# Optimization experiments

Measured on AMD Instinct MI355X. Metric: run time of the kernel, lower is better.

## Reference

```python
import jax, jax.numpy as jnp
import numpy as np

B, T, K, U, C, M, H = 64, 600, 10, 64, 54, 20, 512
OUT = 1 + 6 * M        # 121
IN1 = 3 + C            # 57  -> rnn_cell1 input
IN2 = 3 + C + H        # 569 -> rnn_cell2 input
BIAS = 0.0
EPS = 1e-20


def setup_inputs() -> dict:
    key = jax.random.key(0)
    ks = jax.random.split(key, 20)
    p = lambda k, shape: (jax.random.normal(k, shape, dtype=jnp.float32) * 0.05)
    return {
        "x": jax.random.normal(ks[0], (B, T, 3), dtype=jnp.float32),
        "y": jax.random.uniform(ks[1], (B, T, 3), dtype=jnp.float32),
        "c_vec": jax.random.uniform(ks[2], (B, U, C), dtype=jnp.float32),
        "W_ih1": p(ks[3], (4 * H, IN1)), "W_hh1": p(ks[4], (4 * H, H)),
        "b_ih1": p(ks[5], (4 * H,)),     "b_hh1": p(ks[6], (4 * H,)),
        "W_ih2": p(ks[7], (4 * H, IN2)), "W_hh2": p(ks[8], (4 * H, H)),
        "b_ih2": p(ks[9], (4 * H,)),     "b_hh2": p(ks[10], (4 * H,)),
        "W_k": p(ks[11], (3 * K, H)),    "b_k": p(ks[12], (3 * K,)),
        "W_o": p(ks[13], (OUT, H)),      "b_o": p(ks[14], (OUT,)),
    }


def _lstm_cell(xin, h, c, Wih, Whh, bih, bhh):
    g = xin @ Wih.T + h @ Whh.T + bih + bhh          # [B, 4H]
    i, f, gg, o = jnp.split(g, 4, axis=1)            # PyTorch LSTMCell gate order
    c = jax.nn.sigmoid(f) * c + jax.nn.sigmoid(i) * jnp.tanh(gg)
    h = jax.nn.sigmoid(o) * jnp.tanh(c)
    return h, c


def _forward(x, y, c_vec, W_ih1, W_hh1, b_ih1, b_hh1, W_ih2, W_hh2, b_ih2, b_hh2,
             W_k, b_k, W_o, b_o):
    u = jnp.arange(U, dtype=jnp.float32)[None, None, :]   # [1,1,U]
    zB = jnp.zeros((B, H), dtype=x.dtype)

    def step(carry, xt):
        h1, c1, h2, c2, w, kappa = carry
        h1, c1 = _lstm_cell(jnp.concatenate([xt, w], 1), h1, c1, W_ih1, W_hh1, b_ih1, b_hh1)
        kg = h1 @ W_k.T + b_k                               # [B, 3K]
        a_hat, be_hat, ka_hat = jnp.split(kg, 3, axis=1)
        alpha = jnp.exp(a_hat)[:, :, None]                  # [B,K,1]
        beta = jnp.exp(be_hat)[:, :, None]
        kappa = kappa + jnp.exp(ka_hat)[:, :, None]
        phi = jnp.sum(jnp.exp(-beta * (kappa - u) ** 2) * alpha, axis=1)  # [B,U]
        w = jnp.einsum('bu,buc->bc', phi, c_vec)            # [B,C]
        h2, c2 = _lstm_cell(jnp.concatenate([xt, h1, w], 1), h2, c2, W_ih2, W_hh2, b_ih2, b_hh2)
        return (h1, c1, h2, c2, w, kappa), h2

    init = (zB, zB, zB, zB, jnp.zeros((B, C), x.dtype), jnp.zeros((B, K, 1), x.dtype))
    _, h2_seq = jax.lax.scan(step, init, jnp.transpose(x, (1, 0, 2)))   # [T,B,H]
    h2_seq = jnp.transpose(h2_seq, (1, 0, 2)).reshape(-1, H)            # [B*T,H]
    outputs = h2_seq @ W_o.T + b_o                                      # [B*T,OUT]

    y1, y2, s = jnp.moveaxis(y.reshape(-1, 3), 1, 0)                    # each [B*T]
    e = jax.nn.sigmoid(-outputs[:, 0])                                  # 1/(1+exp(o0))
    pi_hat, mu1, mu2, s1_hat, s2_hat, rho_hat = jnp.split(outputs[:, 1:], 6, axis=1)
    pi = jax.nn.softmax(pi_hat, axis=1)
    sigma1 = jnp.exp(s1_hat - BIAS)
    sigma2 = jnp.exp(s2_hat - BIAS)
    rho = jnp.tanh(rho_hat)
    d1 = (y1[:, None] - mu1) / sigma1
    d2 = (y2[:, None] - mu2) / sigma2
    z = d1 ** 2 + d2 ** 2 - 2.0 * rho * d1 * d2
    one_m_r2 = 1.0 - rho ** 2
    gauss = jnp.exp(-z / (2.0 * one_m_r2)) / (2.0 * np.pi * sigma1 * sigma2 * jnp.sqrt(one_m_r2))
    loss_g = jnp.sum(-jnp.log(jnp.sum(pi * gauss, axis=1) + EPS))
    loss_b = jnp.sum(-jnp.log((e + EPS) * s + (1.0 - e + EPS) * (1.0 - s)))
    return (loss_g + loss_b) / (B * T)


def reference(x, y, c_vec, W_ih1, W_hh1, b_ih1, b_hh1, W_ih2, W_hh2, b_ih2, b_hh2,
              W_k, b_k, W_o, b_o):
    return _forward(x, y, c_vec, W_ih1, W_hh1, b_ih1, b_hh1, W_ih2, W_hh2,
                    b_ih2, b_hh2, W_k, b_k, W_o, b_o)
```

## Files before the change

### kernel.cpp

```cpp
#include <hip/hip_runtime.h>
#include <math.h>

typedef _Float16 f16;
typedef _Float16 f16x8 __attribute__((ext_vector_type(8)));
typedef float f32x4 __attribute__((ext_vector_type(4)));
union HU { f16 h; unsigned short u; };

#define NT 512
#define NBLK 160
#define ABE 69632
#define OUTG_OFF 69632
#define LOSS_OFF 77824
#define FLAG_OFF 78080
#define DYN_LDS 132096

__device__ __forceinline__ f16x8 cld16(const void* p) {
  f16x8 r;
  asm volatile("global_load_dwordx4 %0, %1, off sc0 sc1" : "=v"(r) : "v"(p) : "memory");
  return r;
}
__device__ __forceinline__ uint4 cld128u(const void* p) {
  uint4 r;
  asm volatile("global_load_dwordx4 %0, %1, off sc0 sc1"
               : "=v"(r) : "v"(p) : "memory");
  return r;
}
__device__ __forceinline__ unsigned cld32u(const void* p) {
  unsigned r;
  asm volatile("global_load_dword %0, %1, off sc0 sc1" : "=v"(r) : "v"(p) : "memory");
  return r;
}
__device__ __forceinline__ void cst32(void* p, unsigned v) {
  asm volatile("global_store_dword %0, %1, off sc0 sc1" :: "v"(p), "v"(v) : "memory");
}
#define VMWAIT() do { asm volatile("s_waitcnt vmcnt(0)" ::: "memory"); \
                      __builtin_amdgcn_sched_barrier(0); } while (0)

__device__ __forceinline__ float sigm(float v){ return 1.f/(1.f+expf(-v)); }

__device__ __forceinline__ void gbar(unsigned* flags, unsigned target) {
  asm volatile("s_waitcnt vmcnt(0)" ::: "memory");
  __syncthreads();
  if (threadIdx.x == 0) cst32(flags + blockIdx.x, target);
  if (threadIdx.x < 64) {
    bool ok;
    do {
      uint4 vv; vv.x = vv.y = vv.z = vv.w = target;
      if (threadIdx.x < 40) {
        vv = cld128u(flags + threadIdx.x * 4);
        asm volatile("s_waitcnt vmcnt(0)" ::: "memory");
      }
      ok = (vv.x >= target) && (vv.y >= target) && (vv.z >= target) && (vv.w >= target);
    } while (!__all(ok));
  }
  __syncthreads();
}

__device__ __forceinline__ float mix_loss(const float* so, const float* yl, int t, int m) {
  float y1 = yl[t*3+0], y2 = yl[t*3+1], ys = yl[t*3+2];
  float ph = (m < 20) ? so[1+m] : -1e30f;
  float mx = ph;
  #pragma unroll
  for (int d = 16; d >= 1; d >>= 1) mx = fmaxf(mx, __shfl_xor(mx, d));
  float pe = (m < 20) ? expf(ph - mx) : 0.f;
  float ps = pe;
  #pragma unroll
  for (int d = 16; d >= 1; d >>= 1) ps += __shfl_xor(ps, d);
  float contrib = 0.f;
  if (m < 20) {
    float mu1 = so[21+m], mu2 = so[41+m];
    float s1 = expf(so[61+m]), s2 = expf(so[81+m]);
    float rh = tanhf(so[101+m]);
    float d1 = (y1-mu1)/s1, d2 = (y2-mu2)/s2;
    float omr = 1.f - rh*rh;
    float z = d1*d1 + d2*d2 - 2.f*rh*d1*d2;
    float ga = expf(-z/(2.f*omr)) / (6.283185307179586f * s1 * s2 * sqrtf(omr));
    contrib = (pe/ps)*ga;
  }
  float gs = contrib;
  #pragma unroll
  for (int d = 16; d >= 1; d >>= 1) gs += __shfl_xor(gs, d);
  float lg = -logf(gs + 1e-20f);
  float e = 1.f/(1.f + expf(so[0]));
  float lb = -logf((e + 1e-20f)*ys + (1.f - e + 1e-20f)*(1.f - ys));
  return lg + lb;
}

__global__ __launch_bounds__(256) void k_init(float* ws) {
  unsigned* w0 = (unsigned*)ws;
  unsigned* wb = (unsigned*)ws + FLAG_OFF;
  int idx = blockIdx.x*256 + threadIdx.x;
  int str = gridDim.x*256;
  for (int e = idx; e < ABE; e += str) w0[e] = 0u;
  if (idx < NBLK) wb[idx] = 0u;
}

__global__ __launch_bounds__(NT, 1) void kmain(
    const float* __restrict__ x, const float* __restrict__ y, const float* __restrict__ cvec,
    const float* __restrict__ Wih1, const float* __restrict__ Whh1,
    const float* __restrict__ bih1, const float* __restrict__ bhh1,
    const float* __restrict__ Wih2, const float* __restrict__ Whh2,
    const float* __restrict__ bih2, const float* __restrict__ bhh2,
    const float* __restrict__ Wk, const float* __restrict__ bk,
    const float* __restrict__ Wo, const float* __restrict__ bo,
    float* __restrict__ out, float* __restrict__ ws)
{
  extern __shared__ char dsm[];
  const int blk = blockIdx.x, tid = threadIdx.x;
  const int wv = tid >> 6, l = tid & 63;

  f16* AB = (f16*)ws;
  float* outg  = ws + OUTG_OFF;
  float* lossg = ws + LOSS_OFF;
  unsigned* flags = (unsigned*)ws + FLAG_OFF;

  float lreg = 0.f;

  if (blk < 64) {
    f16* wf2 = (f16*)dsm;
    for (int f = tid; f < 2*34*64; f += NT) {
      int nt = f / (34*64), rem = f - nt*34*64, j = rem >> 6, lf = rem & 63;
      int nrow = nt*16 + (lf & 15);
      int R = (nrow >> 3)*512 + blk*8 + (nrow & 7);
      int kbase = j*32 + (lf >> 4)*8;
      #pragma unroll
      for (int e = 0; e < 8; ++e) {
        int k = kbase + e;
        float v = 0.f;
        if (k >= 4 && k < 58)        v = Wih2[R*569 + 515 + (k-4)];
        else if (k >= 58 && k < 61)  v = Wih2[R*569 + (k-58)];
        else if (k >= 64 && k < 576) v = Wih2[R*569 + 3 + (k-64)];
        else if (k >= 576)           v = Whh2[R*512 + (k-576)];
        wf2[f*8 + e] = (f16)v;
      }
    }
  } else if (blk < 96) {
    const int g1i = blk - 64;
    f16* wf1  = (f16*)dsm;
    f16* wofr = (f16*)(dsm + 73728);
    for (int f = tid; f < 4*18*64; f += NT) {
      int nt = f / (18*64), rem = f - nt*18*64, j = rem >> 6, lf = rem & 63;
      int nrow = nt*16 + (lf & 15);
      int R = (nrow >> 4)*512 + g1i*16 + (nrow & 15);
      int kbase = j*32 + (lf >> 4)*8;
      #pragma unroll
      for (int e = 0; e < 8; ++e) {
        int k = kbase + e;
        float v = 0.f;
        if (k < 3)                   v = Wih1[R*57 + k];
        else if (k >= 4 && k < 58)   v = Wih1[R*57 + 3 + (k-4)];
        else if (k >= 64 && k < 576) v = Whh1[R*512 + (k-64)];
        wf1[f*8 + e] = (f16)v;
      }
    }
    for (int f = tid; f < 16*64; f += NT) {
      int j = f >> 6, lf = f & 63;
      int nrow = lf & 15, row = g1i*4 + nrow;
      int kbase = j*32 + (lf >> 4)*8;
      #pragma unroll
      for (int e = 0; e < 8; ++e) {
        float v = (nrow < 4 && row < 121) ? Wo[row*512 + kbase + e] : 0.f;
        wofr[f*8 + e] = (f16)v;
      }
    }
  } else {
    const int b = blk - 96;
    f16*   wk  = (f16*)dsm;
    float* cv  = (float*)(dsm + 31200);
    float* xl  = (float*)(dsm + 45024);
    float* yl  = (float*)(dsm + 52224);
    for (int e = tid; e < 30*512; e += NT) { int j = e >> 9, k = e & 511; wk[j*520 + k] = (f16)Wk[e]; }
    for (int e = tid; e < 3456; e += NT) cv[e] = cvec[b*3456 + e];
    for (int e = tid; e < 1800; e += NT) { xl[e] = x[b*1800+e]; yl[e] = y[b*1800+e]; }
    float* kap = (float*)(dsm + 61152);
    if (tid < 10) kap[tid] = 0.f;
    __syncthreads();
    if (tid == 0) {
      HU h0, h1u, h2u;
      h0.h = (f16)xl[0]; h1u.h = (f16)xl[1]; h2u.h = (f16)xl[2];
      cst32((unsigned*)AB + (b*1088 >> 1),       (unsigned)h0.u | ((unsigned)h1u.u << 16));
      cst32((unsigned*)AB + ((b*1088 + 2) >> 1), (unsigned)h2u.u);
    }
  }

  float bias_g[4] = {0,0,0,0}, bias1a[4] = {0,0,0,0}, bias1b[4] = {0,0,0,0};
  float borow = 0.f;
  float c_st = 0.f, c1a = 0.f, c1b = 0.f;
  if (blk < 64) {
    int pr = tid & 7;
    #pragma unroll
    for (int g = 0; g < 4; ++g) {
      int R = g*512 + blk*8 + pr;
      bias_g[g] = bih2[R] + bhh2[R];
    }
  } else if (blk < 96) {
    int g1i = blk - 64, pr = tid & 7;
    #pragma unroll
    for (int g = 0; g < 4; ++g) {
      int Ra = g*512 + g1i*16 + 2*pr, Rb = Ra + 1;
      bias1a[g] = bih1[Ra] + bhh1[Ra];
      bias1b[g] = bih1[Rb] + bhh1[Rb];
    }
    int r = tid >> 6;
    if (r < 4) { int row = g1i*4 + r; borow = (row < 121) ? bo[row] : 0.f; }
  }

  gbar(flags, 1);

  for (int i = 0; i <= 601; ++i) {
    const f16* __restrict__ Acur = AB + (i & 1)*ABE;
    f16* __restrict__ Anxt = AB + ((i & 1)^1)*ABE;
    unsigned* AnxtW = (unsigned*)Anxt;

    if (blk < 64) {
      if (i >= 1 && i <= 600) {
        f16* wf2 = (f16*)dsm;
        float* part2 = (float*)(dsm + 69632);
        const int mt = wv & 3, kh = wv >> 2;
        const int mA = mt*16 + (l & 15);
        const int kb = (l >> 4)*8;
        const f16* Ap = Acur + mA*1088;
        f32x4 acc0 = {0,0,0,0}, acc1 = {0,0,0,0};
        f16x8 fr[17];
        #pragma unroll
        for (int jj = 0; jj < 17; ++jj) {
          int j = kh*17 + jj;
          fr[jj] = cld16(Ap + j*32 + kb);
        }
        VMWAIT();
        #pragma unroll
        for (int jj = 0; jj < 17; ++jj) {
          int j = kh*17 + jj;
          f16x8 b0 = *(const f16x8*)&wf2[((0*34 + j)*64 + l)*8];
          f16x8 b1 = *(const f16x8*)&wf2[((1*34 + j)*64 + l)*8];
          acc0 = __builtin_amdgcn_mfma_f32_16x16x32_f16(fr[jj], b0, acc0, 0, 0, 0);
          acc1 = __builtin_amdgcn_mfma_f32_16x16x32_f16(fr[jj], b1, acc1, 0, 0, 0);
        }
        #pragma unroll
        for (int r = 0; r < 4; ++r) {
          int m = mt*16 + (l>>4)*4 + r;
          part2[(kh*64 + m)*33 + (l & 15)]      = acc0[r];
          part2[(kh*64 + m)*33 + 16 + (l & 15)] = acc1[r];
        }
        __syncthreads();
        {
          int b_ = tid >> 3, pr = tid & 7;
          const float* p0 = &part2[(0*64 + b_)*33];
          const float* p1 = &part2[(1*64 + b_)*33];
          float gi_ = p0[0*8+pr] + p1[0*8+pr] + bias_g[0];
          float gf_ = p0[1*8+pr] + p1[1*8+pr] + bias_g[1];
          float gg_ = p0[2*8+pr] + p1[2*8+pr] + bias_g[2];
          float go_ = p0[3*8+pr] + p1[3*8+pr] + bias_g[3];
          float ig = sigm(gi_), fg = sigm(gf_), gg2 = tanhf(gg_), og = sigm(go_);
          c_st = fg*c_st + ig*gg2;
          HU hu; hu.h = (f16)(og * tanhf(c_st));
          unsigned myv = hu.u;
          unsigned other = (unsigned)__shfl_xor((int)myv, 1);
          if ((pr & 1) == 0)
            cst32(AnxtW + ((b_*1088 + 576 + blk*8 + pr) >> 1), myv | (other << 16));
        }
      }
    } else if (blk < 96) {
      const int g1i = blk - 64;
      f16* wf1  = (f16*)dsm;
      f16* wofr = (f16*)(dsm + 73728);
      float* part1 = (float*)(dsm + 90112);
      float* partp = (float*)(dsm + 123392);
      bool do_g1 = (i <= 599), do_pr = (i >= 2);
      const int mt = wv & 3, kh = wv >> 2;
      const int mA = mt*16 + (l & 15);
      const int kb = (l >> 4)*8;
      f16x8 fr1[9], frp[8];
      if (do_g1) {
        const f16* Ap = Acur + mA*1088;
        #pragma unroll
        for (int jj = 0; jj < 9; ++jj) {
          int j = kh*9 + jj;
          fr1[jj] = cld16(Ap + j*32 + kb);
        }
      }
      if (do_pr) {
        const f16* Ap = Acur + mA*1088 + 576;
        #pragma unroll
        for (int jj = 0; jj < 8; ++jj) {
          int j = kh*8 + jj;
          frp[jj] = cld16(Ap + j*32 + kb);
        }
      }
      VMWAIT();
      if (do_g1) {
        f32x4 acc[4];
        #pragma unroll
        for (int nt = 0; nt < 4; ++nt) acc[nt] = (f32x4){0,0,0,0};
        #pragma unroll
        for (int jj = 0; jj < 9; ++jj) {
          int j = kh*9 + jj;
          #pragma unroll
          for (int nt = 0; nt < 4; ++nt) {
            f16x8 bf = *(const f16x8*)&wf1[((nt*18 + j)*64 + l)*8];
            acc[nt] = __builtin_amdgcn_mfma_f32_16x16x32_f16(fr1[jj], bf, acc[nt], 0, 0, 0);
          }
        }
        #pragma unroll
        for (int nt = 0; nt < 4; ++nt)
          #pragma unroll
          for (int r = 0; r < 4; ++r) {
            int m = mt*16 + (l>>4)*4 + r;
            part1[(kh*64 + m)*65 + nt*16 + (l & 15)] = acc[nt][r];
          }
      }
      if (do_pr) {
        f32x4 accp = {0,0,0,0};
        #pragma unroll
        for (int jj = 0; jj < 8; ++jj) {
          int j = kh*8 + jj;
          f16x8 bf = *(const f16x8*)&wofr[(j*64 + l)*8];
          accp = __builtin_amdgcn_mfma_f32_16x16x32_f16(frp[jj], bf, accp, 0, 0, 0);
        }
        #pragma unroll
        for (int r = 0; r < 4; ++r) {
          int m = mt*16 + (l>>4)*4 + r;
          partp[(kh*64 + m)*17 + (l & 15)] = accp[r];
        }
      }
      if (do_g1 || do_pr) __syncthreads();
      if (do_g1) {
        int b_ = tid >> 3, pr = tid & 7;
        const float* p0 = &part1[(0*64 + b_)*65];
        const float* p1 = &part1[(1*64 + b_)*65];
        float giA = p0[0*16+2*pr] + p1[0*16+2*pr] + bias1a[0];
        float gfA = p0[1*16+2*pr] + p1[1*16+2*pr] + bias1a[1];
        float ggA = p0[2*16+2*pr] + p1[2*16+2*pr] + bias1a[2];
        float goA = p0[3*16+2*pr] + p1[3*16+2*pr] + bias1a[3];
        c1a = sigm(gfA)*c1a + sigm(giA)*tanhf(ggA);
        float hA = sigm(goA) * tanhf(c1a);
        float giB = p0[0*16+2*pr+1] + p1[0*16+2*pr+1] + bias1b[0];
        float gfB = p0[1*16+2*pr+1] + p1[1*16+2*pr+1] + bias1b[1];
        float ggB = p0[2*16+2*pr+1] + p1[2*16+2*pr+1] + bias1b[2];
        float goB = p0[3*16+2*pr+1] + p1[3*16+2*pr+1] + bias1b[3];
        c1b = sigm(gfB)*c1b + sigm(giB)*tanhf(ggB);
        float hB = sigm(goB) * tanhf(c1b);
        HU ua, ub; ua.h = (f16)hA; ub.h = (f16)hB;
        cst32(AnxtW + ((b_*1088 + 64 + g1i*16 + 2*pr) >> 1),
              (unsigned)ua.u | ((unsigned)ub.u << 16));
      }
      if (do_pr && tid < 256) {
        int b_ = tid & 63, r = tid >> 6;
        int row = g1i*4 + r;
        if (row < 121) {
          float v = partp[(0*64 + b_)*17 + r] + partp[(1*64 + b_)*17 + r] + borow;
          unsigned uu; __builtin_memcpy(&uu, &v, 4);
          cst32((unsigned*)outg + b_*128 + row, uu);
        }
      }
    }
    gbar(flags, 2 + 2*i);

    if (blk >= 96) {
      const int b = blk - 96;
      f16*   wk   = (f16*)dsm;
      float* cv   = (float*)(dsm + 31200);
      float* xl   = (float*)(dsm + 45024);
      float* yl   = (float*)(dsm + 52224);
      f16*   h1h  = (f16*)(dsm + 59424);
      float* so   = (float*)(dsm + 60448);
      float* skg  = (float*)(dsm + 60944);
      float* sal  = (float*)(dsm + 61072);
      float* sbe  = (float*)(dsm + 61112);
      float* kap  = (float*)(dsm + 61152);
      float* sphi = (float*)(dsm + 61192);
      float* wtmp = (float*)(dsm + 61448);
      if (i <= 599) {
        if (tid < 64) {
          f16x8 hv = cld16(Anxt + b*1088 + 64 + tid*8);
          asm volatile("s_waitcnt vmcnt(0)" ::: "memory");
          *(f16x8*)&h1h[tid*8] = hv;
        }
        __syncthreads();
        {
          int j = tid >> 4, ksv = tid & 15;
          float a = 0.f;
          if (j < 30) {
            const f16* wr = &wk[j*520 + ksv*32];
            const f16* hr = &h1h[ksv*32];
            #pragma unroll
            for (int c = 0; c < 4; ++c) {
              f16x8 q = *(const f16x8*)(wr + c*8);
              f16x8 h = *(const f16x8*)(hr + c*8);
              #pragma unroll
              for (int e = 0; e < 8; ++e) a += (float)q[e] * (float)h[e];
            }
          }
          a += __shfl_xor(a, 1); a += __shfl_xor(a, 2);
          a += __shfl_xor(a, 4); a += __shfl_xor(a, 8);
          if (j < 30 && ksv == 0) skg[j] = a + bk[j];
        }
        __syncthreads();
        if (tid < 10) {
          sal[tid] = expf(skg[tid]);
          sbe[tid] = expf(skg[10+tid]);
          kap[tid] += expf(skg[20+tid]);
        }
        __syncthreads();
        if (tid < 64) {
          float u = (float)tid, ph = 0.f;
          #pragma unroll
          for (int k2 = 0; k2 < 10; ++k2) {
            float d = kap[k2] - u;
            ph += sal[k2]*expf(-sbe[k2]*d*d);
          }
          sphi[tid] = ph;
        }
        __syncthreads();
        if (tid < 54) {
          float wvv = 0.f;
          #pragma unroll 8
          for (int u = 0; u < 64; ++u) wvv += sphi[u]*cv[u*54 + tid];
          wtmp[tid] = wvv;
        }
        __syncthreads();
        if (tid < 27) {
          HU a, bu; a.h = (f16)wtmp[2*tid]; bu.h = (f16)wtmp[2*tid+1];
          cst32(AnxtW + ((b*1088 + 4 + 2*tid) >> 1), (unsigned)a.u | ((unsigned)bu.u << 16));
        } else if (tid == 27) {
          HU a, bu; a.h = (f16)xl[i*3+0]; bu.h = (f16)xl[i*3+1];
          cst32(AnxtW + ((b*1088 + 58) >> 1), (unsigned)a.u | ((unsigned)bu.u << 16));
        } else if (tid == 28) {
          HU a; a.h = (f16)xl[i*3+2];
          cst32(AnxtW + ((b*1088 + 60) >> 1), (unsigned)a.u);
        } else if (tid == 29 && i <= 598) {
          HU a, bu; a.h = (f16)xl[(i+1)*3+0]; bu.h = (f16)xl[(i+1)*3+1];
          cst32(AnxtW + ((b*1088) >> 1), (unsigned)a.u | ((unsigned)bu.u << 16));
        } else if (tid == 30 && i <= 598) {
          HU a; a.h = (f16)xl[(i+1)*3+2];
          cst32(AnxtW + ((b*1088 + 2) >> 1), (unsigned)a.u);
        }
      }
      if (i >= 2) {
        if (tid < 121) {
          unsigned uu = cld32u((unsigned*)outg + b*128 + tid);
          asm volatile("s_waitcnt vmcnt(0)" ::: "memory");
          float v; __builtin_memcpy(&v, &uu, 4);
          so[tid] = v;
        }
        __syncthreads();
        if (tid < 32) {
          float v = mix_loss(so, yl, i-2, tid);
          if (tid == 0) lreg += v;
        }
      }
    }
    gbar(flags, 3 + 2*i);
  }

  if (blk >= 96 && tid == 0) {
    unsigned uu; __builtin_memcpy(&uu, &lreg, 4);
    cst32((unsigned*)lossg + (blk - 96), uu);
  }
  gbar(flags, 1206);
  if (blk == 96 && tid < 64) {
    unsigned uu = cld32u((unsigned*)lossg + tid);
    asm volatile("s_waitcnt vmcnt(0)" ::: "memory");
    float v; __builtin_memcpy(&v, &uu, 4);
    #pragma unroll
    for (int d = 32; d >= 1; d >>= 1) v += __shfl_xor(v, d);
    if (tid == 0) out[0] = v / 38400.f;
  }
}

extern "C" void kernel_launch(void* const* d_in, const int* in_sizes, int n_in,
                              void* d_out, int out_size, void* d_ws, size_t ws_size,
                              hipStream_t stream)
{
  (void)in_sizes; (void)n_in; (void)out_size; (void)ws_size;
  const float* x    = (const float*)d_in[0];
  const float* y    = (const float*)d_in[1];
  const float* cvec = (const float*)d_in[2];
  const float* Wih1 = (const float*)d_in[3];
  const float* Whh1 = (const float*)d_in[4];
  const float* bih1 = (const float*)d_in[5];
  const float* bhh1 = (const float*)d_in[6];
  const float* Wih2 = (const float*)d_in[7];
  const float* Whh2 = (const float*)d_in[8];
  const float* bih2 = (const float*)d_in[9];
  const float* bhh2 = (const float*)d_in[10];
  const float* Wk   = (const float*)d_in[11];
  const float* bk   = (const float*)d_in[12];
  const float* Wo   = (const float*)d_in[13];
  const float* bo   = (const float*)d_in[14];
  float* out = (float*)d_out;
  float* wsf = (float*)d_ws;

  hipFuncSetAttribute((const void*)kmain, hipFuncAttributeMaxDynamicSharedMemorySize, DYN_LDS);

  k_init<<<256, 256, 0, stream>>>(wsf);

  void* args[] = {
    (void*)&x, (void*)&y, (void*)&cvec,
    (void*)&Wih1, (void*)&Whh1, (void*)&bih1, (void*)&bhh1,
    (void*)&Wih2, (void*)&Whh2, (void*)&bih2, (void*)&bhh2,
    (void*)&Wk, (void*)&bk, (void*)&Wo, (void*)&bo,
    (void*)&out, (void*)&wsf
  };
  hipLaunchCooperativeKernel((void*)kmain, dim3(NBLK), dim3(NT), args, DYN_LDS, stream);
}
```

Before: 12.01 ms.

## Repartition persistent LSTM kernel into fewer blocks with register-resident weights

The persistent kernel is remapped from 160 blocks to 89. Eight blocks each own 64 hidden units of LSTM1, sixteen own 32 units of LSTM2, and one block handles the output projection; weights now stay in VGPR fragments instead of LDS. After each grid barrier the recurrent h vectors are staged into LDS, and the gate nonlinearity is computed in registers with lane shuffles, which removes the split-K partial sums and the LDS reduction. Barrier polling uses 64-bit atomic loads, and the projection output is double-buffered. The aim is less barrier fan-in and cheaper per-step work, at the cost of heavy register pressure and more serial MFMA work per block.

```diff
diff --git a/kernel.cpp b/kernel.cpp
--- a/kernel.cpp
+++ b/kernel.cpp
@@ -5,52 +5,58 @@
 typedef _Float16 f16x8 __attribute__((ext_vector_type(8)));
 typedef float f32x4 __attribute__((ext_vector_type(4)));
 union HU { f16 h; unsigned short u; };
+union AFU { unsigned long long q[2]; f16x8 v; };
 
 #define NT 512
-#define NBLK 160
+#define NG1 8
+#define G2B 8
+#define NG2 16
+#define PRB 24
+#define ATB 25
+#define NBLK 89
 #define ABE 69632
+#define ABEH 69632
 #define OUTG_OFF 69632
-#define LOSS_OFF 77824
-#define FLAG_OFF 78080
-#define DYN_LDS 132096
-
-__device__ __forceinline__ f16x8 cld16(const void* p) {
-  f16x8 r;
-  asm volatile("global_load_dwordx4 %0, %1, off sc0 sc1" : "=v"(r) : "v"(p) : "memory");
-  return r;
-}
-__device__ __forceinline__ uint4 cld128u(const void* p) {
-  uint4 r;
-  asm volatile("global_load_dwordx4 %0, %1, off sc0 sc1"
-               : "=v"(r) : "v"(p) : "memory");
-  return r;
-}
-__device__ __forceinline__ unsigned cld32u(const void* p) {
-  unsigned r;
-  asm volatile("global_load_dword %0, %1, off sc0 sc1" : "=v"(r) : "v"(p) : "memory");
-  return r;
+#define LOSS_OFF 86016
+#define FLAG_OFF 86144
+#define DYN_LDS 136704
+#define G1LW 520
+#define G2LW 1032
+#define PRLW 520
+
+__device__ __forceinline__ unsigned long long ald64(const void* p) {
+  return __hip_atomic_load((const unsigned long long*)p, __ATOMIC_RELAXED, __HIP_MEMORY_SCOPE_AGENT);
+}
+__device__ __forceinline__ unsigned ald32(const void* p) {
+  return __hip_atomic_load((const unsigned*)p, __ATOMIC_RELAXED, __HIP_MEMORY_SCOPE_AGENT);
 }
 __device__ __forceinline__ void cst32(void* p, unsigned v) {
   asm volatile("global_store_dword %0, %1, off sc0 sc1" :: "v"(p), "v"(v) : "memory");
 }
+__device__ __forceinline__ void cst128h(void* p, f16x8 v) {
+  asm volatile("global_store_dwordx4 %0, %1, off sc0 sc1" :: "v"(p), "v"(v) : "memory");
+}
+__device__ __forceinline__ void cst128f(void* p, f32x4 v) {
+  asm volatile("global_store_dwordx4 %0, %1, off sc0 sc1" :: "v"(p), "v"(v) : "memory");
+}
 #define VMWAIT() do { asm volatile("s_waitcnt vmcnt(0)" ::: "memory"); \
                       __builtin_amdgcn_sched_barrier(0); } while (0)
 
 __device__ __forceinline__ float sigm(float v){ return 1.f/(1.f+expf(-v)); }
 
 __device__ __forceinline__ void gbar(unsigned* flags, unsigned target) {
-  asm volatile("s_waitcnt vmcnt(0)" ::: "memory");
+  VMWAIT();
   __syncthreads();
   if (threadIdx.x == 0) cst32(flags + blockIdx.x, target);
   if (threadIdx.x < 64) {
     bool ok;
     do {
-      uint4 vv; vv.x = vv.y = vv.z = vv.w = target;
-      if (threadIdx.x < 40) {
-        vv = cld128u(flags + threadIdx.x * 4);
-        asm volatile("s_waitcnt vmcnt(0)" ::: "memory");
-      }
-      ok = (vv.x >= target) && (vv.y >= target) && (vv.z >= target) && (vv.w >= target);
+      unsigned lo = target, hi = target;
+      if (threadIdx.x < 48) {
+        unsigned long long v = ald64(flags + threadIdx.x * 2);
+        lo = (unsigned)v; hi = (unsigned)(v >> 32);
+      }
+      ok = (lo >= target) && (hi >= target);
     } while (!__all(ok));
   }
   __syncthreads();
@@ -88,11 +94,12 @@
 
 __global__ __launch_bounds__(256) void k_init(float* ws) {
   unsigned* w0 = (unsigned*)ws;
-  unsigned* wb = (unsigned*)ws + FLAG_OFF;
+  unsigned* fl = (unsigned*)ws + FLAG_OFF;
   int idx = blockIdx.x*256 + threadIdx.x;
   int str = gridDim.x*256;
   for (int e = idx; e < ABE; e += str) w0[e] = 0u;
-  if (idx < NBLK) wb[idx] = 0u;
+  for (int e = idx; e < 2*8192 + 64; e += str) w0[OUTG_OFF + e] = 0u;
+  if (idx < 96) fl[idx] = (idx < NBLK) ? 0u : 0x7fffffffu;
 }
 
 __global__ __launch_bounds__(NT, 1) void kmain(
@@ -108,63 +115,80 @@
   extern __shared__ char dsm[];
   const int blk = blockIdx.x, tid = threadIdx.x;
   const int wv = tid >> 6, l = tid & 63;
+  const int q = l & 3;
 
   f16* AB = (f16*)ws;
   float* outg  = ws + OUTG_OFF;
   float* lossg = ws + LOSS_OFF;
   unsigned* flags = (unsigned*)ws + FLAG_OFF;
 
-  float lreg = 0.f;
-
-  if (blk < 64) {
-    f16* wf2 = (f16*)dsm;
-    for (int f = tid; f < 2*34*64; f += NT) {
-      int nt = f / (34*64), rem = f - nt*34*64, j = rem >> 6, lf = rem & 63;
-      int nrow = nt*16 + (lf & 15);
-      int R = (nrow >> 3)*512 + blk*8 + (nrow & 7);
-      int kbase = j*32 + (lf >> 4)*8;
+  f16x8 Bf[36];
+  f32x4 acc[8];
+  float cst[32];
+  float bi[2] = {0.f, 0.f};
+  float bpr = 0.f, lreg = 0.f;
+  #pragma unroll
+  for (int z = 0; z < 32; ++z) cst[z] = 0.f;
+
+  if (blk < NG1) {
+    auto wg1 = [&](int R, int k)->float {
+      if (k < 3) return Wih1[R*57 + k];
+      if (k >= 4 && k < 58) return Wih1[R*57 + 3 + (k-4)];
+      if (k >= 64 && k < 576) return Whh1[R*512 + (k-64)];
+      return 0.f;
+    };
+    #pragma unroll
+    for (int nt = 0; nt < 2; ++nt) {
+      int T = wv*2 + nt;
+      int n = T*16 + (l & 15);
+      int R = (n & 3)*512 + blk*64 + (n >> 2);
       #pragma unroll
-      for (int e = 0; e < 8; ++e) {
-        int k = kbase + e;
-        float v = 0.f;
-        if (k >= 4 && k < 58)        v = Wih2[R*569 + 515 + (k-4)];
-        else if (k >= 58 && k < 61)  v = Wih2[R*569 + (k-58)];
-        else if (k >= 64 && k < 576) v = Wih2[R*569 + 3 + (k-64)];
-        else if (k >= 576)           v = Whh2[R*512 + (k-576)];
-        wf2[f*8 + e] = (f16)v;
-      }
+      for (int j = 0; j < 18; ++j) {
+        f16x8 v;
+        #pragma unroll
+        for (int e = 0; e < 8; ++e) v[e] = (f16)wg1(R, j*32 + (l >> 4)*8 + e);
+        Bf[nt*18 + j] = v;
+      }
+      bi[nt] = bih1[R] + bhh1[R];
     }
-  } else if (blk < 96) {
-    const int g1i = blk - 64;
-    f16* wf1  = (f16*)dsm;
-    f16* wofr = (f16*)(dsm + 73728);
-    for (int f = tid; f < 4*18*64; f += NT) {
-      int nt = f / (18*64), rem = f - nt*18*64, j = rem >> 6, lf = rem & 63;
-      int nrow = nt*16 + (lf & 15);
-      int R = (nrow >> 4)*512 + g1i*16 + (nrow & 15);
-      int kbase = j*32 + (lf >> 4)*8;
+    unsigned* z = (unsigned*)dsm;
+    for (int e = tid; e < 64*G1LW/2; e += NT) z[e] = 0u;
+  } else if (blk < G2B + NG2) {
+    const int g2i = blk - G2B;
+    auto wg2 = [&](int R, int k)->float {
+      if (k >= 4 && k < 58) return Wih2[R*569 + 515 + (k-4)];
+      if (k >= 58 && k < 61) return Wih2[R*569 + (k-58)];
+      if (k >= 64 && k < 576) return Wih2[R*569 + 3 + (k-64)];
+      if (k >= 576) return Whh2[R*512 + (k-576)];
+      return 0.f;
+    };
+    int n = wv*16 + (l & 15);
+    int R = (n & 3)*512 + g2i*32 + (n >> 2);
+    #pragma unroll
+    for (int j = 0; j < 34; ++j) {
+      f16x8 v;
       #pragma unroll
-      for (int e = 0; e < 8; ++e) {
-        int k = kbase + e;
-        float v = 0.f;
-        if (k < 3)                   v = Wih1[R*57 + k];
-        else if (k >= 4 && k < 58)   v = Wih1[R*57 + 3 + (k-4)];
-        else if (k >= 64 && k < 576) v = Whh1[R*512 + (k-64)];
-        wf1[f*8 + e] = (f16)v;
-      }
+      for (int e = 0; e < 8; ++e) v[e] = (f16)wg2(R, j*32 + (l >> 4)*8 + e);
+      Bf[j] = v;
     }
-    for (int f = tid; f < 16*64; f += NT) {
-      int j = f >> 6, lf = f & 63;
-      int nrow = lf & 15, row = g1i*4 + nrow;
-      int kbase = j*32 + (lf >> 4)*8;
+    bi[0] = bih2[R] + bhh2[R];
+    unsigned* z = (unsigned*)dsm;
+    for (int e = tid; e < 64*G2LW/2; e += NT) z[e] = 0u;
+  } else if (blk == PRB) {
+    int o = wv*16 + (l & 15);
+    #pragma unroll
+    for (int j = 0; j < 16; ++j) {
+      f16x8 v;
       #pragma unroll
-      for (int e = 0; e < 8; ++e) {
-        float v = (nrow < 4 && row < 121) ? Wo[row*512 + kbase + e] : 0.f;
-        wofr[f*8 + e] = (f16)v;
-      }
+      for (int e = 0; e < 8; ++e)
+        v[e] = (o < 121) ? (f16)Wo[o*512 + j*32 + (l >> 4)*8 + e] : (f16)0.f;
+      Bf[j] = v;
     }
+    bpr = (o < 121) ? bo[o] : 0.f;
+    unsigned* z = (unsigned*)dsm;
+    for (int e = tid; e < 64*PRLW/2; e += NT) z[e] = 0u;
   } else {
-    const int b = blk - 96;
+    const int b = blk - ATB;
     f16*   wk  = (f16*)dsm;
     float* cv  = (float*)(dsm + 31200);
     float* xl  = (float*)(dsm + 45024);
@@ -183,181 +207,212 @@
     }
   }
 
-  float bias_g[4] = {0,0,0,0}, bias1a[4] = {0,0,0,0}, bias1b[4] = {0,0,0,0};
-  float borow = 0.f;
-  float c_st = 0.f, c1a = 0.f, c1b = 0.f;
-  if (blk < 64) {
-    int pr = tid & 7;
-    #pragma unroll
-    for (int g = 0; g < 4; ++g) {
-      int R = g*512 + blk*8 + pr;
-      bias_g[g] = bih2[R] + bhh2[R];
-    }
-  } else if (blk < 96) {
-    int g1i = blk - 64, pr = tid & 7;
-    #pragma unroll
-    for (int g = 0; g < 4; ++g) {
-      int Ra = g*512 + g1i*16 + 2*pr, Rb = Ra + 1;
-      bias1a[g] = bih1[Ra] + bhh1[Ra];
-      bias1b[g] = bih1[Rb] + bhh1[Rb];
-    }
-    int r = tid >> 6;
-    if (r < 4) { int row = g1i*4 + r; borow = (row < 121) ? bo[row] : 0.f; }
-  }
-
   gbar(flags, 1);
 
   for (int i = 0; i <= 601; ++i) {
-    const f16* __restrict__ Acur = AB + (i & 1)*ABE;
-    f16* __restrict__ Anxt = AB + ((i & 1)^1)*ABE;
+    const f16* __restrict__ Acur = AB + (i & 1)*ABEH;
+    f16* __restrict__ Anxt = AB + ((i & 1)^1)*ABEH;
     unsigned* AnxtW = (unsigned*)Anxt;
 
-    if (blk < 64) {
+    if (blk < NG1) {
+      if (i <= 599) {
+        f16* plds = (f16*)dsm;
+        f16* htr  = (f16*)(dsm + 66560);
+        #pragma unroll
+        for (int z = 0; z < 8; ++z) acc[z] = (f32x4){0,0,0,0};
+        const int kb = (l >> 4)*8;
+        AFU a01[4][2];
+        #pragma unroll
+        for (int mt = 0; mt < 4; ++mt)
+          #pragma unroll
+          for (int jd = 0; jd < 2; ++jd) {
+            const f16* bp = Acur + ((l&15) + 16*mt)*1088 + jd*32 + kb;
+            a01[mt][jd].q[0] = ald64(bp);
+            a01[mt][jd].q[1] = ald64(bp + 4);
+          }
+        #pragma unroll
+        for (int j = 2; j < 18; ++j)
+          #pragma unroll
+          for (int mt = 0; mt < 4; ++mt) {
+            f16x8 af = *(const f16x8*)&plds[((l&15) + 16*mt)*G1LW + (j*32 - 64) + kb];
+            #pragma unroll
+            for (int nt = 0; nt < 2; ++nt)
+              acc[nt*4+mt] = __builtin_amdgcn_mfma_f32_16x16x32_f16(af, Bf[nt*18+j], acc[nt*4+mt], 0,0,0);
+          }
+        #pragma unroll
+        for (int mt = 0; mt < 4; ++mt)
+          #pragma unroll
+          for (int jd = 0; jd < 2; ++jd)
+            #pragma unroll
+            for (int nt = 0; nt < 2; ++nt)
+              acc[nt*4+mt] = __builtin_amdgcn_mfma_f32_16x16x32_f16(a01[mt][jd].v, Bf[nt*18+jd], acc[nt*4+mt], 0,0,0);
+        #pragma unroll
+        for (int nt = 0; nt < 2; ++nt) {
+          int dloc = (wv*2 + nt)*4 + ((l & 15) >> 2);
+          #pragma unroll
+          for (int mt = 0; mt < 4; ++mt)
+            #pragma unroll
+            for (int r = 0; r < 4; ++r) {
+              float xme = acc[nt*4+mt][r] + bi[nt];
+              float a1 = __shfl_xor(xme, 1), a2 = __shfl_xor(xme, 2), a3 = __shfl_xor(a1, 2);
+              float gi = q==0?xme: q==1?a1 : q==2?a2 : a3;
+              float gf = q==0?a1 : q==1?xme: q==2?a3 : a2;
+              float gg = q==0?a2 : q==1?a3 : q==2?xme: a1;
+              float go = q==0?a3 : q==1?a2 : q==2?a1 : xme;
+              float c = cst[(nt*4+mt)*4 + r];
+              c = sigm(gf)*c + sigm(gi)*tanhf(gg);
+              cst[(nt*4+mt)*4 + r] = c;
+              float h = sigm(go)*tanhf(c);
+              if (q == 0) htr[(mt*16 + (l>>4)*4 + r)*64 + dloc] = (f16)h;
+            }
+        }
+        __syncthreads();
+        { int m = tid >> 3, qq = tid & 7;
+          f16x8 hv = *(const f16x8*)&htr[m*64 + qq*8];
+          cst128h(Anxt + m*1088 + 64 + blk*64 + qq*8, hv); }
+      }
+    } else if (blk < G2B + NG2) {
       if (i >= 1 && i <= 600) {
-        f16* wf2 = (f16*)dsm;
-        float* part2 = (float*)(dsm + 69632);
-        const int mt = wv & 3, kh = wv >> 2;
-        const int mA = mt*16 + (l & 15);
+        const int g2i = blk - G2B;
+        f16* plds = (f16*)dsm;
+        f16* htr  = (f16*)(dsm + 132096);
+        #pragma unroll
+        for (int z = 0; z < 4; ++z) acc[z] = (f32x4){0,0,0,0};
         const int kb = (l >> 4)*8;
-        const f16* Ap = Acur + mA*1088;
-        f32x4 acc0 = {0,0,0,0}, acc1 = {0,0,0,0};
-        f16x8 fr[17];
-        #pragma unroll
-        for (int jj = 0; jj < 17; ++jj) {
-          int j = kh*17 + jj;
-          fr[jj] = cld16(Ap + j*32 + kb);
-        }
-        VMWAIT();
-        #pragma unroll
-        for (int jj = 0; jj < 17; ++jj) {
-          int j = kh*17 + jj;
-          f16x8 b0 = *(const f16x8*)&wf2[((0*34 + j)*64 + l)*8];
-          f16x8 b1 = *(const f16x8*)&wf2[((1*34 + j)*64 + l)*8];
-          acc0 = __builtin_amdgcn_mfma_f32_16x16x32_f16(fr[jj], b0, acc0, 0, 0, 0);
-          acc1 = __builtin_amdgcn_mfma_f32_16x16x32_f16(fr[jj], b1, acc1, 0, 0, 0);
-        }
-        #pragma unroll
-        for (int r = 0; r < 4; ++r) {
-          int m = mt*16 + (l>>4)*4 + r;
-          part2[(kh*64 + m)*33 + (l & 15)]      = acc0[r];
-          part2[(kh*64 + m)*33 + 16 + (l & 15)] = acc1[r];
-        }
-        __syncthreads();
+        AFU a01[4][2];
+        #pragma unroll
+        for (int mt = 0; mt < 4; ++mt)
+          #pragma unroll
+          for (int jd = 0; jd < 2; ++jd) {
+            const f16* bp = Acur + ((l&15) + 16*mt)*1088 + jd*32 + kb;
+            a01[mt][jd].q[0] = ald64(bp);
+            a01[mt][jd].q[1] = ald64(bp + 4);
+          }
+        #pragma unroll
+        for (int j = 2; j < 34; ++j)
+          #pragma unroll
+          for (int mt = 0; mt < 4; ++mt) {
+            f16x8 af = *(const f16x8*)&plds[((l&15) + 16*mt)*G2LW + (j*32 - 64) + kb];
+            acc[mt] = __builtin_amdgcn_mfma_f32_16x16x32_f16(af, Bf[j], acc[mt], 0,0,0);
+          }
+        #pragma unroll
+        for (int mt = 0; mt < 4; ++mt)
+          #pragma unroll
+          for (int jd = 0; jd < 2; ++jd)
+            acc[mt] = __builtin_amdgcn_mfma_f32_16x16x32_f16(a01[mt][jd].v, Bf[jd], acc[mt], 0,0,0);
         {
-          int b_ = tid >> 3, pr = tid & 7;
-          const float* p0 = &part2[(0*64 + b_)*33];
-          const float* p1 = &part2[(1*64 + b_)*33];
-          float gi_ = p0[0*8+pr] + p1[0*8+pr] + bias_g[0];
-          float gf_ = p0[1*8+pr] + p1[1*8+pr] + bias_g[1];
-          float gg_ = p0[2*8+pr] + p1[2*8+pr] + bias_g[2];
-          float go_ = p0[3*8+pr] + p1[3*8+pr] + bias_g[3];
-          float ig = sigm(gi_), fg = sigm(gf_), gg2 = tanhf(gg_), og = sigm(go_);
-          c_st = fg*c_st + ig*gg2;
-          HU hu; hu.h = (f16)(og * tanhf(c_st));
-          unsigned myv = hu.u;
-          unsigned other = (unsigned)__shfl_xor((int)myv, 1);
-          if ((pr & 1) == 0)
-            cst32(AnxtW + ((b_*1088 + 576 + blk*8 + pr) >> 1), myv | (other << 16));
-        }
-      }
-    } else if (blk < 96) {
-      const int g1i = blk - 64;
-      f16* wf1  = (f16*)dsm;
-      f16* wofr = (f16*)(dsm + 73728);
-      float* part1 = (float*)(dsm + 90112);
-      float* partp = (float*)(dsm + 123392);
-      bool do_g1 = (i <= 599), do_pr = (i >= 2);
-      const int mt = wv & 3, kh = wv >> 2;
-      const int mA = mt*16 + (l & 15);
-      const int kb = (l >> 4)*8;
-      f16x8 fr1[9], frp[8];
-      if (do_g1) {
-        const f16* Ap = Acur + mA*1088;
-        #pragma unroll
-        for (int jj = 0; jj < 9; ++jj) {
-          int j = kh*9 + jj;
-          fr1[jj] = cld16(Ap + j*32 + kb);
-        }
-      }
-      if (do_pr) {
-        const f16* Ap = Acur + mA*1088 + 576;
-        #pragma unroll
-        for (int jj = 0; jj < 8; ++jj) {
-          int j = kh*8 + jj;
-          frp[jj] = cld16(Ap + j*32 + kb);
-        }
-      }
-      VMWAIT();
-      if (do_g1) {
-        f32x4 acc[4];
-        #pragma unroll
-        for (int nt = 0; nt < 4; ++nt) acc[nt] = (f32x4){0,0,0,0};
-        #pragma unroll
-        for (int jj = 0; jj < 9; ++jj) {
-          int j = kh*9 + jj;
-          #pragma unroll
-          for (int nt = 0; nt < 4; ++nt) {
-            f16x8 bf = *(const f16x8*)&wf1[((nt*18 + j)*64 + l)*8];
-            acc[nt] = __builtin_amdgcn_mfma_f32_16x16x32_f16(fr1[jj], bf, acc[nt], 0, 0, 0);
-          }
-        }
-        #pragma unroll
-        for (int nt = 0; nt < 4; ++nt)
-          #pragma unroll
-          for (int r = 0; r < 4; ++r) {
-            int m = mt*16 + (l>>4)*4 + r;
-            part1[(kh*64 + m)*65 + nt*16 + (l & 15)] = acc[nt][r];
-          }
-      }
-      if (do_pr) {
-        f32x4 accp = {0,0,0,0};
-        #pragma unroll
-        for (int jj = 0; jj < 8; ++jj) {
-          int j = kh*8 + jj;
-          f16x8 bf = *(const f16x8*)&wofr[(j*64 + l)*8];
-          accp = __builtin_amdgcn_mfma_f32_16x16x32_f16(frp[jj], bf, accp, 0, 0, 0);
-        }
-        #pragma unroll
-        for (int r = 0; r < 4; ++r) {
-          int m = mt*16 + (l>>4)*4 + r;
-          partp[(kh*64 + m)*17 + (l & 15)] = accp[r];
-        }
-      }
-      if (do_g1 || do_pr) __syncthreads();
-      if (do_g1) {
-        int b_ = tid >> 3, pr = tid & 7;
-        const float* p0 = &part1[(0*64 + b_)*65];
-        const float* p1 = &part1[(1*64 + b_)*65];
-        float giA = p0[0*16+2*pr] + p1[0*16+2*pr] + bias1a[0];
-        float gfA = p0[1*16+2*pr] + p1[1*16+2*pr] + bias1a[1];
-        float ggA = p0[2*16+2*pr] + p1[2*16+2*pr] + bias1a[2];
-        float goA = p0[3*16+2*pr] + p1[3*16+2*pr] + bias1a[3];
-        c1a = sigm(gfA)*c1a + sigm(giA)*tanhf(ggA);
-        float hA = sigm(goA) * tanhf(c1a);
-        float giB = p0[0*16+2*pr+1] + p1[0*16+2*pr+1] + bias1b[0];
-        float gfB = p0[1*16+2*pr+1] + p1[1*16+2*pr+1] + bias1b[1];
-        float ggB = p0[2*16+2*pr+1] + p1[2*16+2*pr+1] + bias1b[2];
-        float goB = p0[3*16+2*pr+1] + p1[3*16+2*pr+1] + bias1b[3];
-        c1b = sigm(gfB)*c1b + sigm(giB)*tanhf(ggB);
-        float hB = sigm(goB) * tanhf(c1b);
-        HU ua, ub; ua.h = (f16)hA; ub.h = (f16)hB;
-        cst32(AnxtW + ((b_*1088 + 64 + g1i*16 + 2*pr) >> 1),
-              (unsigned)ua.u | ((unsigned)ub.u << 16));
-      }
-      if (do_pr && tid < 256) {
-        int b_ = tid & 63, r = tid >> 6;
-        int row = g1i*4 + r;
-        if (row < 121) {
-          float v = partp[(0*64 + b_)*17 + r] + partp[(1*64 + b_)*17 + r] + borow;
-          unsigned uu; __builtin_memcpy(&uu, &v, 4);
-          cst32((unsigned*)outg + b_*128 + row, uu);
+          int dloc = wv*4 + ((l & 15) >> 2);
+          #pragma unroll
+          for (int mt = 0; mt < 4; ++mt)
+            #pragma unroll
+            for (int r = 0; r < 4; ++r) {
+              float xme = acc[mt][r] + bi[0];
+              float a1 = __shfl_xor(xme, 1), a2 = __shfl_xor(xme, 2), a3 = __shfl_xor(a1, 2);
+              float gi = q==0?xme: q==1?a1 : q==2?a2 : a3;
+              float gf = q==0?a1 : q==1?xme: q==2?a3 : a2;
+              float gg = q==0?a2 : q==1?a3 : q==2?xme: a1;
+              float go = q==0?a3 : q==1?a2 : q==2?a1 : xme;
+              float c = cst[mt*4 + r];
+              c = sigm(gf)*c + sigm(gi)*tanhf(gg);
+              cst[mt*4 + r] = c;
+              float h = sigm(go)*tanhf(c);
+              if (q == 0) htr[(mt*16 + (l>>4)*4 + r)*32 + dloc] = (f16)h;
+            }
+        }
+        __syncthreads();
+        if (tid < 256) {
+          int m = tid >> 2, qq = tid & 3;
+          f16x8 hv = *(const f16x8*)&htr[m*32 + qq*8];
+          cst128h(Anxt + m*1088 + 576 + g2i*32 + qq*8, hv);
         }
       }
     }
     gbar(flags, 2 + 2*i);
 
-    if (blk >= 96) {
-      const int b = blk - 96;
+    if (blk < NG1) {
+      if (i <= 599) {
+        f16* plds = (f16*)dsm;
+        AFU tb[8];
+        #pragma unroll
+        for (int it = 0; it < 8; ++it) {
+          int flat = tid + it*512;
+          const f16* bp = Anxt + (flat >> 6)*1088 + 64 + (flat & 63)*8;
+          tb[it].q[0] = ald64(bp);
+          tb[it].q[1] = ald64(bp + 4);
+        }
+        #pragma unroll
+        for (int it = 0; it < 8; ++it) {
+          int flat = tid + it*512;
+          *(f16x8*)&plds[(flat >> 6)*G1LW + (flat & 63)*8] = tb[it].v;
+        }
+      }
+    } else if (blk < G2B + NG2) {
+      if (i <= 599) {
+        f16* plds = (f16*)dsm;
+        AFU tb[8];
+        #pragma unroll
+        for (int half = 0; half < 2; ++half) {
+          #pragma unroll
+          for (int it = 0; it < 8; ++it) {
+            int flat = tid + (half*8 + it)*512;
+            const f16* bp = Anxt + (flat >> 7)*1088 + 64 + (flat & 127)*8;
+            tb[it].q[0] = ald64(bp);
+            tb[it].q[1] = ald64(bp + 4);
+          }
+          #pragma unroll
+          for (int it = 0; it < 8; ++it) {
+            int flat = tid + (half*8 + it)*512;
+            *(f16x8*)&plds[(flat >> 7)*G2LW + (flat & 127)*8] = tb[it].v;
+          }
+        }
+      }
+    } else if (blk == PRB) {
+      if (i >= 1 && i <= 600) {
+        f16* plds = (f16*)dsm;
+        float* otr = (float*)(dsm + 66560);
+        float* outp = outg + ((i + 1) & 1)*8192;
+        AFU tb[8];
+        #pragma unroll
+        for (int it = 0; it < 8; ++it) {
+          int flat = tid + it*512;
+          const f16* bp = Anxt + (flat >> 6)*1088 + 576 + (flat & 63)*8;
+          tb[it].q[0] = ald64(bp);
+          tb[it].q[1] = ald64(bp + 4);
+        }
+        #pragma unroll
+        for (int it = 0; it < 8; ++it) {
+          int flat = tid + it*512;
+          *(f16x8*)&plds[(flat >> 6)*PRLW + (flat & 63)*8] = tb[it].v;
+        }
+        __syncthreads();
+        #pragma unroll
+        for (int z = 0; z < 4; ++z) acc[z] = (f32x4){0,0,0,0};
+        const int kb = (l >> 4)*8;
+        #pragma unroll
+        for (int j = 0; j < 16; ++j)
+          #pragma unroll
+          for (int mt = 0; mt < 4; ++mt) {
+            f16x8 af = *(const f16x8*)&plds[((l&15) + 16*mt)*PRLW + j*32 + kb];
+            acc[mt] = __builtin_amdgcn_mfma_f32_16x16x32_f16(af, Bf[j], acc[mt], 0,0,0);
+          }
+        { int o = wv*16 + (l & 15);
+          #pragma unroll
+          for (int mt = 0; mt < 4; ++mt)
+            #pragma unroll
+            for (int r = 0; r < 4; ++r)
+              otr[(mt*16 + (l>>4)*4 + r)*128 + o] = acc[mt][r] + bpr;
+        }
+        __syncthreads();
+        #pragma unroll
+        for (int it = 0; it < 4; ++it) {
+          int flat = tid + it*512;
+          int m = flat >> 5, o4 = flat & 31;
+          f32x4 v4 = *(const f32x4*)&otr[m*128 + o4*4];
+          cst128f(outp + m*128 + o4*4, v4);
+        }
+      }
+    } else {
+      const int b = blk - ATB;
       f16*   wk   = (f16*)dsm;
       float* cv   = (float*)(dsm + 31200);
       float* xl   = (float*)(dsm + 45024);
@@ -372,9 +427,11 @@
       float* wtmp = (float*)(dsm + 61448);
       if (i <= 599) {
         if (tid < 64) {
-          f16x8 hv = cld16(Anxt + b*1088 + 64 + tid*8);
-          asm volatile("s_waitcnt vmcnt(0)" ::: "memory");
-          *(f16x8*)&h1h[tid*8] = hv;
+          AFU hv;
+          const f16* bp = Anxt + b*1088 + 64 + tid*8;
+          hv.q[0] = ald64(bp);
+          hv.q[1] = ald64(bp + 4);
+          *(f16x8*)&h1h[tid*8] = hv.v;
         }
         __syncthreads();
         {
@@ -385,10 +442,10 @@
             const f16* hr = &h1h[ksv*32];
             #pragma unroll
             for (int c = 0; c < 4; ++c) {
-              f16x8 q = *(const f16x8*)(wr + c*8);
-              f16x8 h = *(const f16x8*)(hr + c*8);
+              f16x8 qv = *(const f16x8*)(wr + c*8);
+              f16x8 hv = *(const f16x8*)(hr + c*8);
               #pragma unroll
-              for (int e = 0; e < 8; ++e) a += (float)q[e] * (float)h[e];
+              for (int e = 0; e < 8; ++e) a += (float)qv[e] * (float)hv[e];
             }
           }
           a += __shfl_xor(a, 1); a += __shfl_xor(a, 2);
@@ -438,8 +495,7 @@
       }
       if (i >= 2) {
         if (tid < 121) {
-          unsigned uu = cld32u((unsigned*)outg + b*128 + tid);
-          asm volatile("s_waitcnt vmcnt(0)" ::: "memory");
+          unsigned uu = ald32((unsigned*)(outg + (i & 1)*8192) + b*128 + tid);
           float v; __builtin_memcpy(&v, &uu, 4);
           so[tid] = v;
         }
@@ -453,14 +509,13 @@
     gbar(flags, 3 + 2*i);
   }
 
-  if (blk >= 96 && tid == 0) {
+  if (blk >= ATB && tid == 0) {
     unsigned uu; __builtin_memcpy(&uu, &lreg, 4);
-    cst32((unsigned*)lossg + (blk - 96), uu);
+    cst32((unsigned*)lossg + (blk - ATB), uu);
   }
   gbar(flags, 1206);
-  if (blk == 96 && tid < 64) {
-    unsigned uu = cld32u((unsigned*)lossg + tid);
-    asm volatile("s_waitcnt vmcnt(0)" ::: "memory");
+  if (blk == ATB && tid < 64) {
+    unsigned uu = ald32((unsigned*)lossg + tid);
     float v; __builtin_memcpy(&v, &uu, 4);
     #pragma unroll
     for (int d = 32; d >= 1; d >>= 1) v += __shfl_xor(v, d);
```

After: 19.98 ms. 1.66x slower.
